# Optimization experiments

Hardware: AMD Instinct MI355X
Metric: run time of the kernel (lower is better)

The kernel has to match this reference:

```python
import jax, jax.numpy as jnp
import numpy as np

N_BUILDINGS = 4096
NUM_CLUSTERS = 128
EMBED_DIM = 128
TEMPORAL_DIM = 24


def setup_inputs() -> dict:
    key = jax.random.key(0)
    ks = jax.random.split(key, 12)
    E, N, C, T = EMBED_DIM, N_BUILDINGS, NUM_CLUSTERS, TEMPORAL_DIM

    def lin(k, fi, fo):
        k1, k2 = jax.random.split(k)
        w = jax.random.normal(k1, (fo, fi), jnp.float32) / np.sqrt(fi).astype(np.float32)
        b = jax.random.normal(k2, (fo,), jnp.float32) * 0.01
        return w, b

    fp_w1, fp_b1 = lin(ks[0], 2 * E + 2, 128)
    fp_w2, fp_b2 = lin(ks[1], 128, 64)
    fp_w3, fp_b3 = lin(ks[2], 64, 1)
    en_w1, en_b1 = lin(ks[3], 1, 16)
    en_w2, en_b2 = lin(ks[4], 16, 1)
    ps_w1, ps_b1 = lin(ks[5], E, 32)
    ps_w2, ps_b2 = lin(ks[6], 32, 1)

    embeddings = jax.random.normal(ks[7], (1, N, E), jnp.float32)
    generation = jax.random.uniform(ks[8], (1, N, T), jnp.float32) * 50.0
    consumption = jax.random.uniform(ks[9], (1, N, T), jnp.float32) * 50.0
    positions = jax.random.uniform(ks[10], (1, N, 2), jnp.float32) * 1000.0
    cluster_assignments = (jnp.arange(N) % C)[None, :].astype(jnp.int32)

    return dict(embeddings=embeddings, generation=generation, consumption=consumption,
                positions=positions,
                fp_w1=fp_w1, fp_b1=fp_b1, fp_w2=fp_w2, fp_b2=fp_b2, fp_w3=fp_w3, fp_b3=fp_b3,
                en_w1=en_w1, en_b1=en_b1, en_w2=en_w2, en_b2=en_b2,
                ps_w1=ps_w1, ps_b1=ps_b1, ps_w2=ps_w2, ps_b2=ps_b2,
                cluster_assignments=cluster_assignments, num_clusters=C, current_hour=12)


def _greedy_cluster(net0, prio, effm, pf):
    """Greedy allocation within one cluster. net0,prio: [K]; effm,pf: [K,K].
    Surplus rows and deficit cols are both visited in descending priority order;
    non-surplus rows have avail=0 and non-deficit cols have needed<=0, matching the
    original code's subset selection + break/continue semantics."""
    K = net0.shape[0]
    order = jnp.argsort(-prio)
    inv = jnp.argsort(order)
    net_o = net0[order]
    eff_o = effm[order][:, order]
    pf_o = pf[order][:, order]

    def outer(dnet, i):
        avail0 = jnp.maximum(net_o[i], 0.0)  # surplus net is never mutated

        def inner(carry, j):
            avail, dn = carry
            needed = -dn[j]
            active = (avail > 0.0) & (needed > 0.0)
            f = jnp.where(active, jnp.minimum(jnp.minimum(avail, needed), pf_o[i, j]), 0.0)
            dn = dn.at[j].add(f * eff_o[i, j])  # deficit receives delivered flow
            return (avail - f, dn), (f, active)

        (_, dnet), (frow, arow) = jax.lax.scan(inner, (avail0, dnet), jnp.arange(K))
        return dnet, (frow, arow)

    dnet, (flows_o, act_o) = jax.lax.scan(outer, net_o, jnp.arange(K))
    return flows_o[inv][:, inv], act_o[inv][:, inv], dnet[inv]


def _forward(embeddings, generation, consumption, positions,
             fp_w1, fp_b1, fp_w2, fp_b2, fp_w3, fp_b3,
             en_w1, en_b1, en_w2, en_b2,
             ps_w1, ps_b1, ps_w2, ps_b2,
             cluster_assignments, num_clusters, current_hour):
    B, N, E = embeddings.shape
    C = num_clusters
    K = N // C
    net = generation[0, :, current_hour] - consumption[0, :, current_hour]  # [N]

    g = jnp.argsort(cluster_assignments[0]).reshape(C, K)  # [C,K] building ids per cluster
    emb_c = embeddings[0][g]   # [C,K,E]
    pos_c = positions[0][g]    # [C,K,2]
    net_c = net[g]             # [C,K]

    # priority scorer (eval mode)
    h = jax.nn.relu(emb_c @ ps_w1.T + ps_b1)
    prio_c = jax.nn.sigmoid(h @ ps_w2.T + ps_b2)[..., 0]  # [C,K]

    # pairwise distances within cluster
    dist = jnp.linalg.norm(pos_c[:, :, None, :] - pos_c[:, None, :, :], axis=-1)  # [C,K,K]

    # efficiency net: eff = 0.85 + 0.13*sigmoid(MLP(dist/1000))
    eh = jax.nn.relu((dist / 1000.0)[..., None] * en_w1[:, 0] + en_b1)  # [C,K,K,16]
    eff = 0.85 + 0.13 * jax.nn.sigmoid(eh @ en_w2.T + en_b2)[..., 0]    # [C,K,K]

    # flow predictor on concat([emb_i, emb_j, dist, hour/24]); split W1 to avoid
    # materializing the [C,K,K,2E+2] feature tensor. Dropout is eval-mode identity.
    W1a, W1b = fp_w1[:, :E], fp_w1[:, E:2 * E]
    w1d, w1h = fp_w1[:, 2 * E], fp_w1[:, 2 * E + 1]
    hi = emb_c @ W1a.T  # [C,K,128]
    hj = emb_c @ W1b.T  # [C,K,128]
    hour_f = current_hour / 24.0
    h1 = jax.nn.relu(hi[:, :, None, :] + hj[:, None, :, :] + dist[..., None] * w1d + hour_f * w1h + fp_b1)
    h2 = jax.nn.relu(h1 @ fp_w2.T + fp_b2)
    pflow = jax.nn.softplus(h2 @ fp_w3.T + fp_b3)[..., 0]  # [C,K,K]

    flows_c, act_c, dnet_c = jax.vmap(_greedy_cluster)(net_c, prio_c, eff, pflow)

    sharing = jnp.zeros((N, N), embeddings.dtype).at[g[:, :, None], g[:, None, :]].set(flows_c)
    effmat = jnp.ones((N, N), embeddings.dtype).at[g[:, :, None], g[:, None, :]].set(
        jnp.where(act_c, eff, 1.0))
    net_after = jnp.zeros((N,), embeddings.dtype).at[g].set(dnet_c)

    sharing = sharing[None]
    effmat = effmat[None]
    total_shared = sharing.sum()
    energy_sent = sharing.sum(axis=2)
    energy_received = (sharing * effmat).sum(axis=1)
    return sharing, effmat, total_shared, energy_sent, energy_received, net_after[None]


def reference(embeddings, generation, consumption, positions,
              fp_w1, fp_b1, fp_w2, fp_b2, fp_w3, fp_b3,
              en_w1, en_b1, en_w2, en_b2,
              ps_w1, ps_b1, ps_w2, ps_b2,
              cluster_assignments, num_clusters, current_hour):
    return _forward(embeddings, generation, consumption, positions,
                    fp_w1, fp_b1, fp_w2, fp_b2, fp_w3, fp_b3,
                    en_w1, en_b1, en_w2, en_b2,
                    ps_w1, ps_b1, ps_w2, ps_b2,
                    cluster_assignments, num_clusters, current_hour)
```

## Files before the change

kernel.cpp:

```cpp
#include <hip/hip_runtime.h>
#include <math.h>

#define NB 4096
#define NC 128
#define NK 32
#define NE 128

typedef __bf16 bf16x8 __attribute__((ext_vector_type(8)));
typedef float floatx4 __attribute__((ext_vector_type(4)));

__device__ __forceinline__ float sigmoidf_(float x){
  if (x >= 0.f){ float z = expf(-x); return 1.f/(1.f+z); }
  float z = expf(x); return z/(1.f+z);
}
__device__ __forceinline__ float softplusf_(float x){
  return fmaxf(x, 0.f) + log1pf(expf(-fabsf(x)));
}
__device__ __forceinline__ unsigned int pack_bf16(float a, float b){
  unsigned short ua = __builtin_bit_cast(unsigned short, (__bf16)a);
  unsigned short ub = __builtin_bit_cast(unsigned short, (__bf16)b);
  return (unsigned int)ua | ((unsigned int)ub << 16);
}

__global__ void k_prep_group(const float* __restrict__ fp_w1, const float* __restrict__ ps_w1,
                             const float* __restrict__ fp_b1, const float* __restrict__ fp_w2,
                             const int* __restrict__ assign, const int* __restrict__ hourp,
                             float* __restrict__ w1at, float* __restrict__ w1bt,
                             float* __restrict__ ps_w1t, int* __restrict__ g,
                             int* __restrict__ row_of, float* __restrict__ w1d_c,
                             float* __restrict__ bzc, unsigned int* __restrict__ w2b,
                             float* __restrict__ total){
  int bid = blockIdx.x;
  int t = threadIdx.x;
  if (bid < 80){
    int idx = bid*256 + t;
    if (idx < 128*128){
      int o = idx >> 7, e = idx & 127;
      w1at[e*128 + o] = fp_w1[o*258 + e];
      w1bt[e*128 + o] = fp_w1[o*258 + 128 + e];
    } else {
      int i2 = idx - 128*128;
      if (i2 < 128*32){
        int e = i2 >> 5, q = i2 & 31;
        ps_w1t[e*32 + q] = ps_w1[q*128 + e];
      }
    }
  } else if (bid < 96){
    __shared__ int hist[NC];
    __shared__ int loc[256];
    int start = (bid - 80)*256;
    for (int c = t; c < NC; c += 256) hist[c] = 0;
    __syncthreads();
    for (int j = t; j < start; j += 256) atomicAdd(&hist[assign[j]], 1);
    int i = start + t;
    int c = assign[i];
    loc[t] = c;
    __syncthreads();
    int r = hist[c];
    for (int j = 0; j < 256; ++j) r += (j < t && loc[j] == c) ? 1 : 0;
    if (r >= NK) r = NK - 1;
    g[c*NK + r] = i;
    row_of[i] = c*NK + r;
  } else if (bid == 96){
    if (t < 128){
      float hour_f = (float)hourp[0] / 24.0f;
      w1d_c[t] = fp_w1[t*258 + 256];
      bzc[t]   = fmaf(hour_f, fp_w1[t*258 + 257], fp_b1[t]);
    }
    if (t == 128) total[0] = 0.f;
  } else {
    for (int idx = t; idx < 4096; idx += 256)
      w2b[idx] = pack_bf16(fp_w2[2*idx], fp_w2[2*idx + 1]);
  }
}

__global__ void k_prio(const float* __restrict__ emb, const float* __restrict__ gen,
                       const float* __restrict__ cons, const float* __restrict__ pos,
                       const float* __restrict__ ps_w1t, const float* __restrict__ ps_b1,
                       const float* __restrict__ ps_w2, const float* __restrict__ ps_b2,
                       const int* __restrict__ row_of, const int* __restrict__ hourp,
                       float* __restrict__ net_c, float* __restrict__ prio_c,
                       float* __restrict__ pos_c){
  __shared__ float es[8*128];
  __shared__ float ws[128*32];
  int t = threadIdx.x;
  int i0 = blockIdx.x*8;
  for (int idx = t; idx < 8*128; idx += 256) es[idx] = emb[i0*128 + idx];
  for (int idx = t; idx < 128*32; idx += 256) ws[idx] = ps_w1t[idx];
  __syncthreads();
  int bl = t >> 5, q = t & 31;
  int i = i0 + bl;
  float acc = ps_b1[q];
  const float* er = &es[bl*128];
  for (int e = 0; e < 128; ++e) acc = fmaf(er[e], ws[e*32 + q], acc);
  float v = fmaxf(acc, 0.f) * ps_w2[q];
  for (int m = 16; m >= 1; m >>= 1) v += __shfl_xor(v, m, 32);
  if (q == 0){
    int ck = row_of[i];
    prio_c[ck] = sigmoidf_(v + ps_b2[0]);
    int h = hourp[0];
    net_c[ck] = gen[i*24 + h] - cons[i*24 + h];
    pos_c[2*ck]   = pos[2*i];
    pos_c[2*ck+1] = pos[2*i+1];
  }
}

__global__ void k_hij(const float* __restrict__ emb, const float* __restrict__ w1at,
                      const float* __restrict__ w1bt, const int* __restrict__ row_of,
                      float* __restrict__ hi_c, float* __restrict__ hj_c){
  __shared__ float es[16*132];
  int t = threadIdx.x;
  int i0 = blockIdx.x*16;
  for (int idx = t; idx < 16*128; idx += 256){
    int b = idx >> 7, e = idx & 127;
    es[b*132 + e] = emb[(i0 + b)*128 + e];
  }
  __syncthreads();
  int o = t & 127, half = t >> 7;
  float ai[8], aj[8];
#pragma unroll
  for (int r = 0; r < 8; ++r){ ai[r] = 0.f; aj[r] = 0.f; }
  for (int e = 0; e < 128; e += 4){
    float wa0 = w1at[(e+0)*128 + o], wa1 = w1at[(e+1)*128 + o];
    float wa2 = w1at[(e+2)*128 + o], wa3 = w1at[(e+3)*128 + o];
    float wb0 = w1bt[(e+0)*128 + o], wb1 = w1bt[(e+1)*128 + o];
    float wb2 = w1bt[(e+2)*128 + o], wb3 = w1bt[(e+3)*128 + o];
#pragma unroll
    for (int r = 0; r < 8; ++r){
      float4 ev = *(const float4*)&es[(half*8 + r)*132 + e];
      ai[r] = fmaf(ev.x, wa0, fmaf(ev.y, wa1, fmaf(ev.z, wa2, fmaf(ev.w, wa3, ai[r]))));
      aj[r] = fmaf(ev.x, wb0, fmaf(ev.y, wb1, fmaf(ev.z, wb2, fmaf(ev.w, wb3, aj[r]))));
    }
  }
#pragma unroll
  for (int r = 0; r < 8; ++r){
    int b = i0 + half*8 + r;
    int ck = row_of[b];
    hi_c[ck*128 + o] = ai[r];
    hj_c[ck*128 + o] = aj[r];
  }
}

__global__ __launch_bounds__(256) void k_pflow(
    const float* __restrict__ hi_c, const float* __restrict__ hj_c,
    const float* __restrict__ pos_c, const float* __restrict__ w1d_c,
    const float* __restrict__ bzc, const unsigned int* __restrict__ w2b,
    const float* __restrict__ fp_b2, const float* __restrict__ fp_w3,
    const float* __restrict__ fp_b3, float* __restrict__ pflow){
  __shared__ unsigned int h1s[128*68];
  __shared__ unsigned int w2s[64*68];
  int t = threadIdx.x;
  int blk = blockIdx.x;
  int c = blk >> 3, iblk = blk & 7;
  int i0 = iblk*4;
  for (int idx = t; idx < 4096; idx += 256)
    w2s[(idx >> 6)*68 + (idx & 63)] = w2b[idx];
  {
    int p = t >> 1, h = t & 1;
    int i = i0 + (p >> 5), j = p & 31;
    float xi = pos_c[(c*NK + i)*2 + 0], yi = pos_c[(c*NK + i)*2 + 1];
    float xj = pos_c[(c*NK + j)*2 + 0], yj = pos_c[(c*NK + j)*2 + 1];
    float dx = xi - xj, dy = yi - yj;
    float d = sqrtf(fmaf(dx, dx, dy*dy));
    const float4* hi4 = (const float4*)(hi_c + (c*NK + i)*128) + h*16;
    const float4* hj4 = (const float4*)(hj_c + (c*NK + j)*128) + h*16;
    const float4* wd4 = (const float4*)w1d_c + h*16;
    const float4* bz4 = (const float4*)bzc + h*16;
    unsigned int* dst = &h1s[p*68 + h*32];
#pragma unroll
    for (int z = 0; z < 16; ++z){
      float4 a = hi4[z], b = hj4[z], w = wd4[z], bb = bz4[z];
      float v0 = fmaxf(a.x + b.x + fmaf(d, w.x, bb.x), 0.f);
      float v1 = fmaxf(a.y + b.y + fmaf(d, w.y, bb.y), 0.f);
      float v2 = fmaxf(a.z + b.z + fmaf(d, w.z, bb.z), 0.f);
      float v3 = fmaxf(a.w + b.w + fmaf(d, w.w, bb.w), 0.f);
      dst[2*z]     = pack_bf16(v0, v1);
      dst[2*z + 1] = pack_bf16(v2, v3);
    }
  }
  __syncthreads();
  int lane = t & 63, wv = t >> 6;
  int quad = lane >> 4, l16 = lane & 15;
  bf16x8 bfr[4][4];
#pragma unroll
  for (int nt = 0; nt < 4; ++nt)
#pragma unroll
    for (int ks = 0; ks < 4; ++ks){
      int o = nt*16 + l16;
      bfr[nt][ks] = *(const bf16x8*)((const char*)w2s + o*272 + ks*64 + quad*16);
    }
  float b3 = fp_b3[0];
  float b2v[4], w3v[4];
#pragma unroll
  for (int nt = 0; nt < 4; ++nt){
    b2v[nt] = fp_b2[nt*16 + l16];
    w3v[nt] = fp_w3[nt*16 + l16];
  }
  int idx0 = c*1024 + i0*32;
#pragma unroll
  for (int mt2 = 0; mt2 < 2; ++mt2){
    int mt = wv*2 + mt2;
    bf16x8 af[4];
#pragma unroll
    for (int ks = 0; ks < 4; ++ks){
      int m = mt*16 + l16;
      af[ks] = *(const bf16x8*)((const char*)h1s + m*272 + ks*64 + quad*16);
    }
    floatx4 acc[4];
#pragma unroll
    for (int nt = 0; nt < 4; ++nt){
      acc[nt] = (floatx4){0.f, 0.f, 0.f, 0.f};
#pragma unroll
      for (int ks = 0; ks < 4; ++ks)
        acc[nt] = __builtin_amdgcn_mfma_f32_16x16x32_bf16(af[ks], bfr[nt][ks], acc[nt], 0, 0, 0);
    }
    float s0 = 0.f, s1 = 0.f, s2 = 0.f, s3 = 0.f;
#pragma unroll
    for (int nt = 0; nt < 4; ++nt){
      s0 = fmaf(fmaxf(acc[nt][0] + b2v[nt], 0.f), w3v[nt], s0);
      s1 = fmaf(fmaxf(acc[nt][1] + b2v[nt], 0.f), w3v[nt], s1);
      s2 = fmaf(fmaxf(acc[nt][2] + b2v[nt], 0.f), w3v[nt], s2);
      s3 = fmaf(fmaxf(acc[nt][3] + b2v[nt], 0.f), w3v[nt], s3);
    }
#pragma unroll
    for (int m = 8; m >= 1; m >>= 1){
      s0 += __shfl_xor(s0, m);
      s1 += __shfl_xor(s1, m);
      s2 += __shfl_xor(s2, m);
      s3 += __shfl_xor(s3, m);
    }
    if (l16 == 0){
      int base = idx0 + mt*16 + quad*4;
      pflow[base + 0] = softplusf_(s0 + b3);
      pflow[base + 1] = softplusf_(s1 + b3);
      pflow[base + 2] = softplusf_(s2 + b3);
      pflow[base + 3] = softplusf_(s3 + b3);
    }
  }
}

__global__ __launch_bounds__(64) void k_greedy(
    const float* __restrict__ net_c, const float* __restrict__ prio_c,
    const float* __restrict__ pos_c, const float* __restrict__ en_w1,
    const float* __restrict__ en_b1, const float* __restrict__ en_w2,
    const float* __restrict__ en_b2, const float* __restrict__ pflow,
    const int* __restrict__ g,
    float* __restrict__ fl_c, float* __restrict__ ef_c, float* __restrict__ total,
    float* __restrict__ esent, float* __restrict__ erecv, float* __restrict__ nafter){
  __shared__ float pf_s[1024];
  __shared__ float ef_s[1024];
  __shared__ float fl_s[1024];
  __shared__ float efm_s[1024];
  __shared__ float px[32], py[32];
  __shared__ int order_s[32];
  __shared__ int gl[32];
  int t = threadIdx.x;
  int tl = t & 31;
  int c = blockIdx.x;
  for (int e = t; e < 1024; e += 64) pf_s[e] = pflow[c*1024 + e];
  if (t < 32){
    float2 p2 = ((const float2*)pos_c)[c*NK + t];
    px[t] = p2.x; py[t] = p2.y;
    gl[t] = g[c*NK + t];
  }
  __syncthreads();
  for (int e = t; e < 1024; e += 64){
    int ii = e >> 5, jj = e & 31;
    float dx = px[ii] - px[jj], dy = py[ii] - py[jj];
    float d = sqrtf(fmaf(dx, dx, dy*dy));
    float ds = d * (1.0f/1000.0f);
    float acc = en_b2[0];
#pragma unroll
    for (int q = 0; q < 16; ++q)
      acc = fmaf(fmaxf(fmaf(ds, en_w1[q], en_b1[q]), 0.f), en_w2[q], acc);
    ef_s[e] = 0.85f + 0.13f*sigmoidf_(acc);
  }
  float p = (t < 32) ? prio_c[c*NK + t] : -1e30f;
  int rank = 0;
  for (int k = 0; k < 32; ++k){
    float pk = __shfl(p, k, 32);
    rank += ((pk > p) || (pk == p && k < tl)) ? 1 : 0;
  }
  if (t < 32) order_s[rank] = t;
  __syncthreads();
  int b = order_s[tl];
  float net0 = net_c[c*NK + b];
  float dnet = net0;
  float recv = 0.f;
  float ctotal = 0.f;
  for (int i = 0; i < 32; ++i){
    int a = order_s[i];
    float av0 = fmaxf(__shfl(net0, i, 32), 0.f);
    float pf = pf_s[a*32 + b];
    float ef = ef_s[a*32 + b];
    float needed = -dnet;
    float m = (needed > 0.f) ? fminf(needed, pf) : 0.f;
    float s = m;
#pragma unroll
    for (int dd = 1; dd < 32; dd <<= 1){
      float u = __shfl_up(s, dd, 32);
      if (tl >= dd) s += u;
    }
    float Se = __shfl_up(s, 1, 32);
    if (tl == 0) Se = 0.f;
    float rprev = fmaxf(av0 - Se, 0.f);
    int act = (rprev > 0.f) && (needed > 0.f);
    float f = fminf(m, rprev);
    dnet = fmaf(f, ef, dnet);
    recv = fmaf(f, ef, recv);
    if (t < 32){
      fl_s[a*32 + b]  = f;
      efm_s[a*32 + b] = act ? ef : 1.0f;
    }
    float rs = f;
    for (int mm = 16; mm >= 1; mm >>= 1) rs += __shfl_xor(rs, mm, 32);
    if (t == 0){ esent[gl[a]] = rs; ctotal += rs; }
  }
  if (t < 32){
    nafter[gl[b]] = dnet;
    erecv[gl[b]]  = recv;
  }
  if (t == 0) atomicAdd(total, ctotal);
  __syncthreads();
  for (int e = t; e < 1024; e += 64){
    fl_c[c*1024 + e] = fl_s[e];
    ef_c[c*1024 + e] = efm_s[e];
  }
}

__global__ __launch_bounds__(256) void k_write(
    const float* __restrict__ fl_c, const float* __restrict__ ef_c,
    const int* __restrict__ g, const int* __restrict__ row_of,
    float* __restrict__ sharing, float* __restrict__ effm){
  __shared__ float rowS[4096];
  __shared__ float rowE[4096];
  __shared__ int   cols[32];
  __shared__ float vals[32];
  __shared__ float vale[32];
  int t = threadIdx.x;
  int r = blockIdx.x;
  int ra = row_of[r];
  int c = ra >> 5, a = ra & 31;
  if (t < 32){
    cols[t] = g[c*NK + t];
    vals[t] = fl_c[c*1024 + a*32 + t];
    vale[t] = ef_c[c*1024 + a*32 + t];
  }
  float4 z4 = make_float4(0.f, 0.f, 0.f, 0.f);
  float4 o4 = make_float4(1.f, 1.f, 1.f, 1.f);
  float4* s4 = (float4*)rowS;
  float4* e4 = (float4*)rowE;
#pragma unroll
  for (int q = 0; q < 4; ++q){ s4[t + 256*q] = z4; e4[t + 256*q] = o4; }
  __syncthreads();
  if (t < 32){ rowS[cols[t]] = vals[t]; rowE[cols[t]] = vale[t]; }
  __syncthreads();
  float4* gs = (float4*)(sharing + (long)r*NB);
  float4* ge = (float4*)(effm    + (long)r*NB);
#pragma unroll
  for (int q = 0; q < 4; ++q){ gs[t + 256*q] = s4[t + 256*q]; ge[t + 256*q] = e4[t + 256*q]; }
}

extern "C" void kernel_launch(void* const* d_in, const int* in_sizes, int n_in,
                              void* d_out, int out_size, void* d_ws, size_t ws_size,
                              hipStream_t stream){
  (void)in_sizes; (void)n_in; (void)out_size; (void)ws_size;
  const float* emb   = (const float*)d_in[0];
  const float* gen   = (const float*)d_in[1];
  const float* cons  = (const float*)d_in[2];
  const float* pos   = (const float*)d_in[3];
  const float* fp_w1 = (const float*)d_in[4];
  const float* fp_b1 = (const float*)d_in[5];
  const float* fp_w2 = (const float*)d_in[6];
  const float* fp_b2 = (const float*)d_in[7];
  const float* fp_w3 = (const float*)d_in[8];
  const float* fp_b3 = (const float*)d_in[9];
  const float* en_w1 = (const float*)d_in[10];
  const float* en_b1 = (const float*)d_in[11];
  const float* en_w2 = (const float*)d_in[12];
  const float* en_b2 = (const float*)d_in[13];
  const float* ps_w1 = (const float*)d_in[14];
  const float* ps_b1 = (const float*)d_in[15];
  const float* ps_w2 = (const float*)d_in[16];
  const float* ps_b2 = (const float*)d_in[17];
  const int*   assign = (const int*)d_in[18];
  const int*   hourp  = (const int*)d_in[20];

  char* ws = (char*)d_ws;
  float* w1at   = (float*)(ws + 0);
  float* w1bt   = (float*)(ws + 65536);
  float* ps_w1t = (float*)(ws + 131072);
  int*   g      = (int*)  (ws + 147456);
  int*   row_of = (int*)  (ws + 163840);
  float* net_c  = (float*)(ws + 180224);
  float* prio_c = (float*)(ws + 196608);
  float* pos_c  = (float*)(ws + 212992);
  float* w1d_c  = (float*)(ws + 245760);
  float* bzc    = (float*)(ws + 246272);
  float* hi_c   = (float*)(ws + 262144);
  float* hj_c   = (float*)(ws + 2359296);
  float* pflow  = (float*)(ws + 4456448);
  float* fl_c   = (float*)(ws + 4980736);
  float* ef_c   = (float*)(ws + 5505024);
  unsigned int* w2b = (unsigned int*)(ws + 6029312);

  float* sharing = (float*)d_out;
  float* effm    = sharing + (long)NB*NB;
  float* total   = effm + (long)NB*NB;
  float* esent   = total + 1;
  float* erecv   = esent + NB;
  float* nafter  = erecv + NB;

  hipLaunchKernelGGL(k_prep_group, dim3(98), dim3(256), 0, stream,
                     fp_w1, ps_w1, fp_b1, fp_w2, assign, hourp,
                     w1at, w1bt, ps_w1t, g, row_of, w1d_c, bzc, w2b, total);
  hipLaunchKernelGGL(k_prio, dim3(512), dim3(256), 0, stream,
                     emb, gen, cons, pos, ps_w1t, ps_b1, ps_w2, ps_b2,
                     row_of, hourp, net_c, prio_c, pos_c);
  hipLaunchKernelGGL(k_hij, dim3(256), dim3(256), 0, stream,
                     emb, w1at, w1bt, row_of, hi_c, hj_c);
  hipLaunchKernelGGL(k_pflow, dim3(1024), dim3(256), 0, stream,
                     hi_c, hj_c, pos_c, w1d_c, bzc, w2b, fp_b2, fp_w3, fp_b3,
                     pflow);
  hipLaunchKernelGGL(k_greedy, dim3(128), dim3(64), 0, stream,
                     net_c, prio_c, pos_c, en_w1, en_b1, en_w2, en_b2, pflow, g,
                     fl_c, ef_c, total, esent, erecv, nafter);
  hipLaunchKernelGGL(k_write, dim3(4096), dim3(256), 0, stream,
                     fl_c, ef_c, g, row_of, sharing, effm);
}
```

Baseline: 274.3 us.

## Build MFMA fragments directly in registers and pre-swizzle W2 to drop LDS staging

The pair-flow kernel no longer stages the first-layer activations and W2 through shared memory. Each wave now computes its own 16-row A fragments straight into registers and loads B fragments from a W2 buffer that the prep kernel pre-arranges in MFMA lane order. This removes the LDS round trip and the block barrier. In exchange, more blocks are launched and each lane makes redundant global reads of hi/hj rows and W2, which should mostly hit cache.

```diff
diff --git a/kernel.cpp b/kernel.cpp
--- a/kernel.cpp
+++ b/kernel.cpp
@@ -28,7 +28,7 @@
                              float* __restrict__ w1at, float* __restrict__ w1bt,
                              float* __restrict__ ps_w1t, int* __restrict__ g,
                              int* __restrict__ row_of, float* __restrict__ w1d_c,
-                             float* __restrict__ bzc, unsigned int* __restrict__ w2b,
+                             float* __restrict__ bzc, uint4* __restrict__ w2f,
                              float* __restrict__ total){
   int bid = blockIdx.x;
   int t = threadIdx.x;
@@ -69,8 +69,19 @@
     }
     if (t == 128) total[0] = 0.f;
   } else {
-    for (int idx = t; idx < 4096; idx += 256)
-      w2b[idx] = pack_bf16(fp_w2[2*idx], fp_w2[2*idx + 1]);
+    for (int ff = t; ff < 1024; ff += 256){
+      int lane = ff & 63, fi = ff >> 6;
+      int nt = fi >> 2, ks = fi & 3;
+      int o = nt*16 + (lane & 15);
+      int kb = ks*32 + (lane >> 4)*8;
+      const float* src = fp_w2 + o*128 + kb;
+      uint4 u;
+      u.x = pack_bf16(src[0], src[1]);
+      u.y = pack_bf16(src[2], src[3]);
+      u.z = pack_bf16(src[4], src[5]);
+      u.w = pack_bf16(src[6], src[7]);
+      w2f[ff] = u;
+    }
   }
 }
 
@@ -144,98 +155,79 @@
 __global__ __launch_bounds__(256) void k_pflow(
     const float* __restrict__ hi_c, const float* __restrict__ hj_c,
     const float* __restrict__ pos_c, const float* __restrict__ w1d_c,
-    const float* __restrict__ bzc, const unsigned int* __restrict__ w2b,
+    const float* __restrict__ bzc, const uint4* __restrict__ w2f,
     const float* __restrict__ fp_b2, const float* __restrict__ fp_w3,
     const float* __restrict__ fp_b3, float* __restrict__ pflow){
-  __shared__ unsigned int h1s[128*68];
-  __shared__ unsigned int w2s[64*68];
-  int t = threadIdx.x;
-  int blk = blockIdx.x;
-  int c = blk >> 3, iblk = blk & 7;
-  int i0 = iblk*4;
-  for (int idx = t; idx < 4096; idx += 256)
-    w2s[(idx >> 6)*68 + (idx & 63)] = w2b[idx];
-  {
-    int p = t >> 1, h = t & 1;
-    int i = i0 + (p >> 5), j = p & 31;
-    float xi = pos_c[(c*NK + i)*2 + 0], yi = pos_c[(c*NK + i)*2 + 1];
-    float xj = pos_c[(c*NK + j)*2 + 0], yj = pos_c[(c*NK + j)*2 + 1];
-    float dx = xi - xj, dy = yi - yj;
-    float d = sqrtf(fmaf(dx, dx, dy*dy));
-    const float4* hi4 = (const float4*)(hi_c + (c*NK + i)*128) + h*16;
-    const float4* hj4 = (const float4*)(hj_c + (c*NK + j)*128) + h*16;
-    const float4* wd4 = (const float4*)w1d_c + h*16;
-    const float4* bz4 = (const float4*)bzc + h*16;
-    unsigned int* dst = &h1s[p*68 + h*32];
-#pragma unroll
-    for (int z = 0; z < 16; ++z){
-      float4 a = hi4[z], b = hj4[z], w = wd4[z], bb = bz4[z];
-      float v0 = fmaxf(a.x + b.x + fmaf(d, w.x, bb.x), 0.f);
-      float v1 = fmaxf(a.y + b.y + fmaf(d, w.y, bb.y), 0.f);
-      float v2 = fmaxf(a.z + b.z + fmaf(d, w.z, bb.z), 0.f);
-      float v3 = fmaxf(a.w + b.w + fmaf(d, w.w, bb.w), 0.f);
-      dst[2*z]     = pack_bf16(v0, v1);
-      dst[2*z + 1] = pack_bf16(v2, v3);
-    }
-  }
-  __syncthreads();
+  int t = threadIdx.x;
   int lane = t & 63, wv = t >> 6;
-  int quad = lane >> 4, l16 = lane & 15;
+  int gw = blockIdx.x*4 + wv;
+  int c = gw >> 6;
+  int rem = gw & 63;
+  int i = rem >> 1, j0 = (rem & 1)*16;
+  int l16 = lane & 15, quad = lane >> 4;
+  int j = j0 + l16;
+  float xi = pos_c[(c*NK + i)*2 + 0], yi = pos_c[(c*NK + i)*2 + 1];
+  float xj = pos_c[(c*NK + j)*2 + 0], yj = pos_c[(c*NK + j)*2 + 1];
+  float dx = xi - xj, dy = yi - yj;
+  float d = sqrtf(fmaf(dx, dx, dy*dy));
+  const float4* hi4 = (const float4*)(hi_c + (c*NK + i)*128);
+  const float4* hj4 = (const float4*)(hj_c + (c*NK + j)*128);
+  const float4* wd4 = (const float4*)w1d_c;
+  const float4* bz4 = (const float4*)bzc;
+  bf16x8 af[4];
+#pragma unroll
+  for (int ks = 0; ks < 4; ++ks){
+    int q8 = ks*8 + quad*2;
+    float4 a0 = hi4[q8], a1 = hi4[q8 + 1];
+    float4 b0 = hj4[q8], b1 = hj4[q8 + 1];
+    float4 w0 = wd4[q8], w1 = wd4[q8 + 1];
+    float4 z0 = bz4[q8], z1 = bz4[q8 + 1];
+    float v0 = fmaxf(a0.x + b0.x + fmaf(d, w0.x, z0.x), 0.f);
+    float v1 = fmaxf(a0.y + b0.y + fmaf(d, w0.y, z0.y), 0.f);
+    float v2 = fmaxf(a0.z + b0.z + fmaf(d, w0.z, z0.z), 0.f);
+    float v3 = fmaxf(a0.w + b0.w + fmaf(d, w0.w, z0.w), 0.f);
+    float v4 = fmaxf(a1.x + b1.x + fmaf(d, w1.x, z1.x), 0.f);
+    float v5 = fmaxf(a1.y + b1.y + fmaf(d, w1.y, z1.y), 0.f);
+    float v6 = fmaxf(a1.z + b1.z + fmaf(d, w1.z, z1.z), 0.f);
+    float v7 = fmaxf(a1.w + b1.w + fmaf(d, w1.w, z1.w), 0.f);
+    uint4 u;
+    u.x = pack_bf16(v0, v1);
+    u.y = pack_bf16(v2, v3);
+    u.z = pack_bf16(v4, v5);
+    u.w = pack_bf16(v6, v7);
+    af[ks] = __builtin_bit_cast(bf16x8, u);
+  }
   bf16x8 bfr[4][4];
 #pragma unroll
   for (int nt = 0; nt < 4; ++nt)
 #pragma unroll
-    for (int ks = 0; ks < 4; ++ks){
-      int o = nt*16 + l16;
-      bfr[nt][ks] = *(const bf16x8*)((const char*)w2s + o*272 + ks*64 + quad*16);
-    }
-  float b3 = fp_b3[0];
+    for (int ks = 0; ks < 4; ++ks)
+      bfr[nt][ks] = __builtin_bit_cast(bf16x8, w2f[(nt*4 + ks)*64 + lane]);
+  floatx4 acc[4];
+#pragma unroll
+  for (int nt = 0; nt < 4; ++nt){
+    acc[nt] = (floatx4){0.f, 0.f, 0.f, 0.f};
+#pragma unroll
+    for (int ks = 0; ks < 4; ++ks)
+      acc[nt] = __builtin_amdgcn_mfma_f32_16x16x32_bf16(af[ks], bfr[nt][ks], acc[nt], 0, 0, 0);
+  }
   float b2v[4], w3v[4];
 #pragma unroll
   for (int nt = 0; nt < 4; ++nt){
     b2v[nt] = fp_b2[nt*16 + l16];
     w3v[nt] = fp_w3[nt*16 + l16];
   }
-  int idx0 = c*1024 + i0*32;
-#pragma unroll
-  for (int mt2 = 0; mt2 < 2; ++mt2){
-    int mt = wv*2 + mt2;
-    bf16x8 af[4];
-#pragma unroll
-    for (int ks = 0; ks < 4; ++ks){
-      int m = mt*16 + l16;
-      af[ks] = *(const bf16x8*)((const char*)h1s + m*272 + ks*64 + quad*16);
-    }
-    floatx4 acc[4];
-#pragma unroll
-    for (int nt = 0; nt < 4; ++nt){
-      acc[nt] = (floatx4){0.f, 0.f, 0.f, 0.f};
-#pragma unroll
-      for (int ks = 0; ks < 4; ++ks)
-        acc[nt] = __builtin_amdgcn_mfma_f32_16x16x32_bf16(af[ks], bfr[nt][ks], acc[nt], 0, 0, 0);
-    }
-    float s0 = 0.f, s1 = 0.f, s2 = 0.f, s3 = 0.f;
-#pragma unroll
-    for (int nt = 0; nt < 4; ++nt){
-      s0 = fmaf(fmaxf(acc[nt][0] + b2v[nt], 0.f), w3v[nt], s0);
-      s1 = fmaf(fmaxf(acc[nt][1] + b2v[nt], 0.f), w3v[nt], s1);
-      s2 = fmaf(fmaxf(acc[nt][2] + b2v[nt], 0.f), w3v[nt], s2);
-      s3 = fmaf(fmaxf(acc[nt][3] + b2v[nt], 0.f), w3v[nt], s3);
-    }
-#pragma unroll
-    for (int m = 8; m >= 1; m >>= 1){
-      s0 += __shfl_xor(s0, m);
-      s1 += __shfl_xor(s1, m);
-      s2 += __shfl_xor(s2, m);
-      s3 += __shfl_xor(s3, m);
-    }
-    if (l16 == 0){
-      int base = idx0 + mt*16 + quad*4;
-      pflow[base + 0] = softplusf_(s0 + b3);
-      pflow[base + 1] = softplusf_(s1 + b3);
-      pflow[base + 2] = softplusf_(s2 + b3);
-      pflow[base + 3] = softplusf_(s3 + b3);
-    }
+  float b3 = fp_b3[0];
+#pragma unroll
+  for (int r = 0; r < 4; ++r){
+    float s = 0.f;
+#pragma unroll
+    for (int nt = 0; nt < 4; ++nt)
+      s = fmaf(fmaxf(acc[nt][r] + b2v[nt], 0.f), w3v[nt], s);
+#pragma unroll
+    for (int m = 8; m >= 1; m >>= 1) s += __shfl_xor(s, m);
+    if (l16 == 0)
+      pflow[c*1024 + i*32 + j0 + quad*4 + r] = softplusf_(s + b3);
   }
 }
 
@@ -402,7 +394,7 @@
   float* pflow  = (float*)(ws + 4456448);
   float* fl_c   = (float*)(ws + 4980736);
   float* ef_c   = (float*)(ws + 5505024);
-  unsigned int* w2b = (unsigned int*)(ws + 6029312);
+  uint4* w2f    = (uint4*)(ws + 6029312);
 
   float* sharing = (float*)d_out;
   float* effm    = sharing + (long)NB*NB;
@@ -413,14 +405,14 @@
 
   hipLaunchKernelGGL(k_prep_group, dim3(98), dim3(256), 0, stream,
                      fp_w1, ps_w1, fp_b1, fp_w2, assign, hourp,
-                     w1at, w1bt, ps_w1t, g, row_of, w1d_c, bzc, w2b, total);
+                     w1at, w1bt, ps_w1t, g, row_of, w1d_c, bzc, w2f, total);
   hipLaunchKernelGGL(k_prio, dim3(512), dim3(256), 0, stream,
                      emb, gen, cons, pos, ps_w1t, ps_b1, ps_w2, ps_b2,
                      row_of, hourp, net_c, prio_c, pos_c);
   hipLaunchKernelGGL(k_hij, dim3(256), dim3(256), 0, stream,
                      emb, w1at, w1bt, row_of, hi_c, hj_c);
-  hipLaunchKernelGGL(k_pflow, dim3(1024), dim3(256), 0, stream,
-                     hi_c, hj_c, pos_c, w1d_c, bzc, w2b, fp_b2, fp_w3, fp_b3,
+  hipLaunchKernelGGL(k_pflow, dim3(2048), dim3(256), 0, stream,
+                     hi_c, hj_c, pos_c, w1d_c, bzc, w2f, fp_b2, fp_w3, fp_b3,
                      pflow);
   hipLaunchKernelGGL(k_greedy, dim3(128), dim3(64), 0, stream,
                      net_c, prio_c, pos_c, en_w1, en_b1, en_w2, en_b2, pflow, g,
```

Measured after the change: 267.5 us. 1.03x faster.
